# Performance work log

Measured on AMD Instinct MI355X. Metric: run time of the kernel, lower is better.

The kernel has to match this reference:

```python
import jax, jax.numpy as jnp
import numpy as np

CLIP = 10.0  # tanh clipping constant (Kool et al. C=10)


def setup_inputs() -> dict:
    key = jax.random.key(0)
    kq, kk, kv, km = jax.random.split(key, 4)
    B, M, N, D = 16, 2048, 2048, 128
    Q = jax.random.normal(kq, (B, M, D), dtype=jnp.float32)
    K = jax.random.normal(kk, (B, N, D), dtype=jnp.float32)
    V = jax.random.normal(kv, (B, N, D), dtype=jnp.float32)
    # mask: [B, N, 1] bool; True means "forbidden" (set logit to -inf).
    # p=0.3 so every row keeps plenty of valid keys (no all-masked rows).
    mask = jax.random.bernoulli(km, 0.3, (B, N, 1))
    return {"Q": Q, "K": K, "V": V, "mask": mask}


def reference(Q, K, V, mask):
    d_k = jnp.asarray(K.shape[-1], dtype=Q.dtype)
    # logits: [B, M, N]
    logits = jnp.einsum("bmd,bnd->bmn", Q, K) / jnp.sqrt(d_k)
    logits = CLIP * jnp.tanh(logits)
    # mask [B, N, 1] -> [B, 1, N], broadcast over query dim
    mask_t = jnp.transpose(mask, (0, 2, 1))
    logits = jnp.where(mask_t, -jnp.inf, logits)
    probs = jax.nn.softmax(logits, axis=-1)
    return jnp.einsum("bmn,bnd->bmd", probs, V)
```

## Files before the change

kernel.cpp:

```cpp
#include <hip/hip_runtime.h>
#include <hip/hip_fp16.h>

typedef _Float16 h8 __attribute__((ext_vector_type(8)));
typedef _Float16 h4 __attribute__((ext_vector_type(4)));
typedef float f32x4 __attribute__((ext_vector_type(4)));

#define MFMA16(a, b, c) __builtin_amdgcn_mfma_f32_16x16x32_f16((a), (b), (c), 0, 0, 0)

static constexpr int MM = 2048, NN = 2048, DD = 128;
static constexpr int MT = 64, KT = 64, NT = NN / KT;
static constexpr size_t KV_IMG = (size_t)16 * 32 * 16384;
static constexpr size_t WS_NEED = 2 * KV_IMG + 32768 * 4;

static constexpr float C1 = 0.25503487f;
static constexpr float C2 = 28.853900817779268f;
static constexpr float CVALID = 14.426950408889634f;
static constexpr float CMASK = -1.0e30f;

__device__ inline void glds16(const void* g, void* l) {
  __builtin_amdgcn_global_load_lds(
      (const __attribute__((address_space(1))) void*)g,
      (__attribute__((address_space(3))) void*)l, 16, 0, 0);
}

__global__ __launch_bounds__(256) void prep_all(
    const float* __restrict__ K, const float* __restrict__ V,
    const void* __restrict__ mraw, unsigned char* __restrict__ kimg,
    unsigned char* __restrict__ vimg, float* __restrict__ biasC) {
  const int id = blockIdx.x;
  const int tid = threadIdx.x;
  if (id >= 1024) {
    const unsigned int* mw = (const unsigned int*)mraw;
    const unsigned char* mb = (const unsigned char*)mraw;
    int okW = 1;
    for (int w = tid; w < 8192; w += 256) {
      unsigned int v = mw[w];
      okW &= (v == 0u || v == 1u || v == 0x3f800000u) ? 1 : 0;
    }
    __shared__ int sW;
    if (tid == 0) sW = 1;
    __syncthreads();
    if (!okW) atomicAnd(&sW, 0);
    __syncthreads();
    const int i = (id - 1024) * 256 + tid;
    bool masked = sW ? (mw[i] != 0u) : (mb[i] != 0);
    biasC[i] = masked ? CMASK : CVALID;
    return;
  }
  const int bt = id & 511;
  if (id < 512) {
    const float* src = K + (size_t)bt * KT * DD;
    unsigned char* dst = kimg + (size_t)bt * 16384;
#pragma unroll
    for (int it = 0; it < 4; ++it) {
      const int key = (tid >> 4) + 16 * it;
      const int o = tid & 15;
      f32x4 a = *(const f32x4*)(src + key * DD + 8 * o);
      f32x4 c = *(const f32x4*)(src + key * DD + 8 * o + 4);
      h8 hv;
#pragma unroll
      for (int j = 0; j < 4; ++j) {
        hv[j] = (_Float16)a[j];
        hv[j + 4] = (_Float16)c[j];
      }
      *(h8*)(dst + key * 256 + ((16 * o) ^ ((key & 7) << 4))) = hv;
    }
  } else {
    const float* src = V + (size_t)bt * KT * DD;
    unsigned char* dst = vimg + (size_t)bt * 16384;
    const int d = tid & 127;
    const int half = tid >> 7;
#pragma unroll
    for (int ki = 0; ki < 4; ++ki) {
      const int koct = half * 4 + ki;
      h8 w;
#pragma unroll
      for (int q = 0; q < 8; ++q)
        w[q] = (_Float16)src[(8 * koct + q) * DD + d];
      *(h8*)(dst + d * 128 + 16 * (koct ^ ((d >> 1) & 7))) = w;
    }
  }
}

__global__ __launch_bounds__(512, 4) void attn_main(
    const float* __restrict__ Qg, const unsigned char* __restrict__ kimg,
    const unsigned char* __restrict__ vimg, const float* __restrict__ biasC,
    float* __restrict__ out) {
  __shared__ __align__(16) unsigned char smem[76032];
  const int tid = threadIdx.x;
  const int lane = tid & 63;
  const int wv = tid >> 6;
  const int r = lane & 15;
  const int g = lane >> 4;
  const int rw = wv >> 1;
  const int h = wv & 1;
  const int bid = blockIdx.x;
  const int swz = ((bid & 7) << 6) | (bid >> 3);
  const int b = swz >> 5;
  const int mt = swz & 31;
  const int m0 = mt * MT + rw * 16;

  h8 qh[4];
  {
    const float* qr = Qg + ((size_t)b * MM + m0 + r) * DD;
#pragma unroll
    for (int t = 0; t < 4; ++t) {
      f32x4 a = *(const f32x4*)(qr + 32 * t + 8 * g);
      f32x4 c = *(const f32x4*)(qr + 32 * t + 8 * g + 4);
      h8 hi;
#pragma unroll
      for (int j = 0; j < 4; ++j) {
        hi[j] = (_Float16)a[j];
        hi[j + 4] = (_Float16)c[j];
      }
      qh[t] = hi;
    }
  }

  f32x4 acc[8];
#pragma unroll
  for (int cd = 0; cd < 8; ++cd) acc[cd] = (f32x4){0.f, 0.f, 0.f, 0.f};
  float rs[4] = {0.f, 0.f, 0.f, 0.f};

  const unsigned char* kib = kimg + (size_t)b * 32 * 16384;
  const unsigned char* vib = vimg + (size_t)b * 32 * 16384;
  const float* cb = biasC + b * NN;
  _Float16* plds = (_Float16*)(smem + 65536 + wv * 1280);

#pragma unroll
  for (int i = 0; i < 2; ++i) {
    const int off = wv * 2048 + i * 1024;
    glds16(kib + off + lane * 16, smem + off);
    glds16(vib + off + lane * 16, smem + 16384 + off);
  }
  __syncthreads();

  for (int tn = 0; tn < NT; ++tn) {
    const unsigned char* kbuf = smem + (tn & 1) * 32768;
    const unsigned char* vbuf = kbuf + 16384;
    if (tn + 1 < NT) {
      unsigned char* nbuf = smem + ((tn + 1) & 1) * 32768;
      const unsigned char* ks = kib + (size_t)(tn + 1) * 16384;
      const unsigned char* vs = vib + (size_t)(tn + 1) * 16384;
#pragma unroll
      for (int i = 0; i < 2; ++i) {
        const int off = wv * 2048 + i * 1024;
        glds16(ks + off + lane * 16, nbuf + off);
        glds16(vs + off + lane * 16, nbuf + 16384 + off);
      }
    }

#pragma unroll
    for (int c = 0; c < 2; ++c) {
      f32x4 S = {0.f, 0.f, 0.f, 0.f};
      const int key = h * 32 + 16 * c + r;
      const int krow = key << 8;
      const int ksw = (key & 7) << 4;
      __builtin_amdgcn_s_setprio(1);
#pragma unroll
      for (int t = 0; t < 4; ++t) {
        h8 kf = *(const h8*)(kbuf + krow + ((64 * t + 16 * g) ^ ksw));
        S = MFMA16(qh[t], kf, S);
      }
      __builtin_amdgcn_s_setprio(0);
      const float Cc = cb[tn * KT + key];
#pragma unroll
      for (int j = 0; j < 4; ++j) {
        float u = __builtin_amdgcn_exp2f(S[j] * C1);
        float p = __builtin_amdgcn_exp2f(
            fmaf(-C2, __builtin_amdgcn_rcpf(u + 1.0f), Cc));
        rs[j] += p;
        plds[(4 * g + j) * 40 + 16 * c + r] = (_Float16)p;
      }
    }
    h8 a0 = *(const h8*)((unsigned char*)plds + r * 80 + 16 * g);
    __builtin_amdgcn_s_setprio(1);
#pragma unroll
    for (int cd = 0; cd < 8; ++cd) {
      const int d = 16 * cd + r;
      h8 vf = *(const h8*)(vbuf + (d << 7) +
                           ((64 * h + 16 * g) ^ (((d >> 1) & 7) << 4)));
      acc[cd] = MFMA16(a0, vf, acc[cd]);
    }
    __builtin_amdgcn_s_setprio(0);
    __syncthreads();
  }

#pragma unroll
  for (int j = 0; j < 4; ++j) {
    float v = rs[j];
    v += __shfl_xor(v, 1);
    v += __shfl_xor(v, 2);
    v += __shfl_xor(v, 4);
    v += __shfl_xor(v, 8);
    rs[j] = v;
  }

  float* olds = (float*)smem;
  float* rslds = (float*)(smem + 75776);
  if (h == 1) {
    float* my = olds + rw * 2048;
#pragma unroll
    for (int cd = 0; cd < 8; ++cd)
#pragma unroll
      for (int j = 0; j < 4; ++j)
        my[(4 * g + j) * 128 + 16 * cd + r] = acc[cd][j];
    if (r == 0) {
#pragma unroll
      for (int j = 0; j < 4; ++j) rslds[rw * 16 + 4 * g + j] = rs[j];
    }
  }
  __syncthreads();
  if (h == 0) {
    const float* ot = olds + rw * 2048;
    float* ob = out + ((size_t)b * MM + m0) * DD;
#pragma unroll
    for (int j = 0; j < 4; ++j) {
      const int rl = 4 * g + j;
      const float tot = rs[j] + rslds[rw * 16 + rl];
      const float inv = __builtin_amdgcn_rcpf(tot);
#pragma unroll
      for (int cd = 0; cd < 8; ++cd) {
        float v = acc[cd][j] + ot[rl * 128 + 16 * cd + r];
        ob[rl * DD + 16 * cd + r] = v * inv;
      }
    }
  }
}

__global__ __launch_bounds__(256, 2) void attn_fallback(
    const float* __restrict__ Qg, const float* __restrict__ Kg,
    const float* __restrict__ Vg, const float* __restrict__ biasC,
    float* __restrict__ out) {
  __shared__ __align__(16) unsigned char smem[51456];
  const int tid = threadIdx.x;
  const int lane = tid & 63;
  const int wv = tid >> 6;
  const int r = lane & 15;
  const int g = lane >> 4;
  const int rw = wv >> 1;
  const int h = wv & 1;
  const int b = blockIdx.x >> 5;
  const int mt = blockIdx.x & 31;
  const int m0 = mt * MT + rw * 32;

  float* blds = (float*)(smem + 43264);
  {
    const float* cb = biasC + b * NN;
#pragma unroll
    for (int i = 0; i < 8; ++i) blds[tid + 256 * i] = cb[tid + 256 * i];
  }
  h8 qh[2][4];
  {
    const float* qb = Qg + ((size_t)b * MM + m0) * DD;
#pragma unroll
    for (int rf = 0; rf < 2; ++rf) {
      const float* qr = qb + (16 * rf + r) * DD;
#pragma unroll
      for (int t = 0; t < 4; ++t) {
        f32x4 a = *(const f32x4*)(qr + 32 * t + 8 * g);
        f32x4 c = *(const f32x4*)(qr + 32 * t + 8 * g + 4);
        h8 hi;
#pragma unroll
        for (int j = 0; j < 4; ++j) {
          hi[j] = (_Float16)a[j];
          hi[j + 4] = (_Float16)c[j];
        }
        qh[rf][t] = hi;
      }
    }
  }
  f32x4 acc[2][8];
#pragma unroll
  for (int rf = 0; rf < 2; ++rf)
#pragma unroll
    for (int cd = 0; cd < 8; ++cd) acc[rf][cd] = (f32x4){0.f, 0.f, 0.f, 0.f};
  float rs[2][4] = {{0.f, 0.f, 0.f, 0.f}, {0.f, 0.f, 0.f, 0.f}};
  const float* kb = Kg + (size_t)b * NN * DD;
  const float* vbp = Vg + (size_t)b * NN * DD;
  _Float16* plds = (_Float16*)(smem + 32768 + wv * 2560);
  const int bk0 = tid >> 5, bd0 = tid & 31;
  const int bk1 = (256 + tid) >> 5, bd1 = tid & 31;
  f32x4 kpre[8], vpre[8];
#pragma unroll
  for (int i = 0; i < 8; ++i) kpre[i] = *(const f32x4*)(kb + i * 1024 + tid * 4);
#pragma unroll
  for (int q = 0; q < 4; ++q) {
    vpre[q] = *(const f32x4*)(vbp + (4 * bk0 + q) * DD + 4 * bd0);
    vpre[4 + q] = *(const f32x4*)(vbp + (4 * bk1 + q) * DD + 4 * bd1);
  }
  for (int tn = 0; tn < NT; ++tn) {
#pragma unroll
    for (int i = 0; i < 8; ++i) {
      const int flat = i * 1024 + tid * 4;
      const int key = flat >> 7;
      const int d0 = flat & 127;
      h4 hv;
#pragma unroll
      for (int j = 0; j < 4; ++j) hv[j] = (_Float16)kpre[i][j];
      *(h4*)(smem + (key << 8) + ((d0 << 1) ^ ((key & 7) << 4))) = hv;
    }
#pragma unroll
    for (int it = 0; it < 2; ++it) {
      const int bk = it ? bk1 : bk0;
      const int bd = it ? bd1 : bd0;
#pragma unroll
      for (int p = 0; p < 4; ++p) {
        h4 w;
#pragma unroll
        for (int q = 0; q < 4; ++q) w[q] = (_Float16)vpre[it * 4 + q][p];
        const int d = 4 * bd + p;
        *(h4*)(smem + 16384 + (d << 7) +
               ((bk << 3) ^ (((d >> 1) & 7) << 4))) = w;
      }
    }
    if (tn + 1 < NT) {
      const float* ks = kb + (tn + 1) * KT * DD;
      const float* vs = vbp + (tn + 1) * KT * DD;
#pragma unroll
      for (int i = 0; i < 8; ++i) kpre[i] = *(const f32x4*)(ks + i * 1024 + tid * 4);
#pragma unroll
      for (int q = 0; q < 4; ++q) {
        vpre[q] = *(const f32x4*)(vs + (4 * bk0 + q) * DD + 4 * bd0);
        vpre[4 + q] = *(const f32x4*)(vs + (4 * bk1 + q) * DD + 4 * bd1);
      }
    }
    __syncthreads();
#pragma unroll
    for (int c = 0; c < 2; ++c) {
      f32x4 S0 = {0.f, 0.f, 0.f, 0.f}, S1 = {0.f, 0.f, 0.f, 0.f};
      const int key = h * 32 + 16 * c + r;
      const int krow = key << 8;
      const int ksw = (key & 7) << 4;
#pragma unroll
      for (int t = 0; t < 4; ++t) {
        h8 kf = *(const h8*)(smem + krow + ((64 * t + 16 * g) ^ ksw));
        S0 = MFMA16(qh[0][t], kf, S0);
        S1 = MFMA16(qh[1][t], kf, S1);
      }
      const float Cc = blds[tn * KT + key];
#pragma unroll
      for (int j = 0; j < 4; ++j) {
        float u0 = __builtin_amdgcn_exp2f(S0[j] * C1);
        float p0 = __builtin_amdgcn_exp2f(
            fmaf(-C2, __builtin_amdgcn_rcpf(u0 + 1.0f), Cc));
        rs[0][j] += p0;
        plds[(4 * g + j) * 40 + 16 * c + r] = (_Float16)p0;
        float u1 = __builtin_amdgcn_exp2f(S1[j] * C1);
        float p1 = __builtin_amdgcn_exp2f(
            fmaf(-C2, __builtin_amdgcn_rcpf(u1 + 1.0f), Cc));
        rs[1][j] += p1;
        plds[(16 + 4 * g + j) * 40 + 16 * c + r] = (_Float16)p1;
      }
    }
    h8 a0 = *(const h8*)((unsigned char*)plds + r * 80 + 16 * g);
    h8 a1 = *(const h8*)((unsigned char*)plds + (16 + r) * 80 + 16 * g);
#pragma unroll
    for (int cd = 0; cd < 8; ++cd) {
      const int d = 16 * cd + r;
      h8 vf = *(const h8*)(smem + 16384 + (d << 7) +
                           ((64 * h + 16 * g) ^ (((d >> 1) & 7) << 4)));
      acc[0][cd] = MFMA16(a0, vf, acc[0][cd]);
      acc[1][cd] = MFMA16(a1, vf, acc[1][cd]);
    }
    __syncthreads();
  }
#pragma unroll
  for (int rf = 0; rf < 2; ++rf)
#pragma unroll
    for (int j = 0; j < 4; ++j) {
      float v = rs[rf][j];
      v += __shfl_xor(v, 1);
      v += __shfl_xor(v, 2);
      v += __shfl_xor(v, 4);
      v += __shfl_xor(v, 8);
      rs[rf][j] = v;
    }
  float* olds = (float*)smem;
  float* rslds = (float*)(smem + 43008);
  if (h == 1) {
    float* my = olds + rw * 4096;
#pragma unroll
    for (int rf = 0; rf < 2; ++rf)
#pragma unroll
      for (int cd = 0; cd < 8; ++cd)
#pragma unroll
        for (int j = 0; j < 4; ++j)
          my[(16 * rf + 4 * g + j) * 128 + 16 * cd + r] = acc[rf][cd][j];
    if (r == 0) {
#pragma unroll
      for (int rf = 0; rf < 2; ++rf)
#pragma unroll
        for (int j = 0; j < 4; ++j)
          rslds[rw * 32 + 16 * rf + 4 * g + j] = rs[rf][j];
    }
  }
  __syncthreads();
  if (h == 0) {
    const float* ot = olds + rw * 4096;
    float* ob = out + ((size_t)b * MM + m0) * DD;
#pragma unroll
    for (int rf = 0; rf < 2; ++rf)
#pragma unroll
      for (int j = 0; j < 4; ++j) {
        const int rl = 16 * rf + 4 * g + j;
        const float tot = rs[rf][j] + rslds[rw * 32 + rl];
        const float inv = __builtin_amdgcn_rcpf(tot);
#pragma unroll
        for (int cd = 0; cd < 8; ++cd) {
          float v = acc[rf][cd][j] + ot[rl * 128 + 16 * cd + r];
          ob[rl * DD + 16 * cd + r] = v * inv;
        }
      }
  }
}

extern "C" void kernel_launch(void* const* d_in, const int* in_sizes, int n_in,
                              void* d_out, int out_size, void* d_ws, size_t ws_size,
                              hipStream_t stream) {
  const float* Q = (const float*)d_in[0];
  const float* K = (const float*)d_in[1];
  const float* V = (const float*)d_in[2];
  const void* mask = d_in[3];
  float* out = (float*)d_out;
  if (ws_size >= WS_NEED) {
    unsigned char* kimg = (unsigned char*)d_ws;
    unsigned char* vimg = kimg + KV_IMG;
    float* biasC = (float*)(kimg + 2 * KV_IMG);
    prep_all<<<dim3(1152), dim3(256), 0, stream>>>(K, V, mask, kimg, vimg, biasC);
    attn_main<<<dim3(512), dim3(512), 0, stream>>>(Q, kimg, vimg, biasC, out);
  } else {
    float* biasC = (float*)d_ws;
    prep_all<<<dim3(1152), dim3(256), 0, stream>>>(K, V, mask,
        (unsigned char*)d_ws, (unsigned char*)d_ws, biasC);
    attn_fallback<<<dim3(512), dim3(256), 0, stream>>>(Q, K, V, biasC, out);
  }
}
```

Baseline: 81.97 us.

## Switch attention main loop to 32x32x16 MFMA with 4-wave blocks

Rewrites the main attention kernel to use 32x32x16 MFMA tiles: each wave now owns 32 query rows and 32 keys per tile, with 256-thread blocks instead of 512. Row sums are computed with an MFMA against a ones vector instead of cross-lane shuffles, and the V image swizzle changes to match the new read pattern. This aims to cut LDS fragment reads and instruction overhead per FLOP, at the cost of more accumulator registers and fewer waves per block. The fallback path also gets a lighter bias-only prep kernel.

```diff
diff --git a/kernel.cpp b/kernel.cpp
--- a/kernel.cpp
+++ b/kernel.cpp
@@ -4,8 +4,10 @@
 typedef _Float16 h8 __attribute__((ext_vector_type(8)));
 typedef _Float16 h4 __attribute__((ext_vector_type(4)));
 typedef float f32x4 __attribute__((ext_vector_type(4)));
+typedef float f32x16 __attribute__((ext_vector_type(16)));
 
 #define MFMA16(a, b, c) __builtin_amdgcn_mfma_f32_16x16x32_f16((a), (b), (c), 0, 0, 0)
+#define MFMA32(a, b, c) __builtin_amdgcn_mfma_f32_32x32x16_f16((a), (b), (c), 0, 0, 0)
 
 static constexpr int MM = 2048, NN = 2048, DD = 128;
 static constexpr int MT = 64, KT = 64, NT = NN / KT;
@@ -21,6 +23,26 @@
   __builtin_amdgcn_global_load_lds(
       (const __attribute__((address_space(1))) void*)g,
       (__attribute__((address_space(3))) void*)l, 16, 0, 0);
+}
+
+__global__ __launch_bounds__(256) void prep_bias(const void* __restrict__ mraw,
+                                                 float* __restrict__ biasC) {
+  const int tid = threadIdx.x;
+  const unsigned int* mw = (const unsigned int*)mraw;
+  const unsigned char* mb = (const unsigned char*)mraw;
+  int okW = 1;
+  for (int w = tid; w < 8192; w += 256) {
+    unsigned int v = mw[w];
+    okW &= (v == 0u || v == 1u || v == 0x3f800000u) ? 1 : 0;
+  }
+  __shared__ int sW;
+  if (tid == 0) sW = 1;
+  __syncthreads();
+  if (!okW) atomicAnd(&sW, 0);
+  __syncthreads();
+  const int i = blockIdx.x * 256 + tid;
+  bool masked = sW ? (mw[i] != 0u) : (mb[i] != 0);
+  biasC[i] = masked ? CMASK : CVALID;
 }
 
 __global__ __launch_bounds__(256) void prep_all(
@@ -77,12 +99,12 @@
 #pragma unroll
       for (int q = 0; q < 8; ++q)
         w[q] = (_Float16)src[(8 * koct + q) * DD + d];
-      *(h8*)(dst + d * 128 + 16 * (koct ^ ((d >> 1) & 7))) = w;
-    }
-  }
-}
-
-__global__ __launch_bounds__(512, 4) void attn_main(
+      *(h8*)(dst + d * 128 + 16 * (koct ^ (d & 7))) = w;
+    }
+  }
+}
+
+__global__ __launch_bounds__(256, 2) void attn_main(
     const float* __restrict__ Qg, const unsigned char* __restrict__ kimg,
     const unsigned char* __restrict__ vimg, const float* __restrict__ biasC,
     float* __restrict__ out) {
@@ -90,50 +112,63 @@
   const int tid = threadIdx.x;
   const int lane = tid & 63;
   const int wv = tid >> 6;
-  const int r = lane & 15;
-  const int g = lane >> 4;
+  const int l31 = lane & 31;
+  const int hp = lane >> 5;
   const int rw = wv >> 1;
   const int h = wv & 1;
   const int bid = blockIdx.x;
   const int swz = ((bid & 7) << 6) | (bid >> 3);
   const int b = swz >> 5;
   const int mt = swz & 31;
-  const int m0 = mt * MT + rw * 16;
-
-  h8 qh[4];
+  const int m0 = mt * MT + rw * 32;
+
+  h8 qa[8];
   {
-    const float* qr = Qg + ((size_t)b * MM + m0 + r) * DD;
-#pragma unroll
-    for (int t = 0; t < 4; ++t) {
-      f32x4 a = *(const f32x4*)(qr + 32 * t + 8 * g);
-      f32x4 c = *(const f32x4*)(qr + 32 * t + 8 * g + 4);
+    const float* qr = Qg + ((size_t)b * MM + m0 + l31) * DD;
+#pragma unroll
+    for (int st = 0; st < 8; ++st) {
+      const int d0 = 16 * st + 8 * hp;
+      f32x4 a = *(const f32x4*)(qr + d0);
+      f32x4 c = *(const f32x4*)(qr + d0 + 4);
       h8 hi;
 #pragma unroll
       for (int j = 0; j < 4; ++j) {
         hi[j] = (_Float16)a[j];
         hi[j + 4] = (_Float16)c[j];
       }
-      qh[t] = hi;
-    }
-  }
-
-  f32x4 acc[8];
-#pragma unroll
-  for (int cd = 0; cd < 8; ++cd) acc[cd] = (f32x4){0.f, 0.f, 0.f, 0.f};
-  float rs[4] = {0.f, 0.f, 0.f, 0.f};
+      qa[st] = hi;
+    }
+  }
+
+  f32x16 oacc[4];
+  f32x16 rsacc;
+#pragma unroll
+  for (int dc = 0; dc < 4; ++dc)
+#pragma unroll
+    for (int j = 0; j < 16; ++j) oacc[dc][j] = 0.f;
+#pragma unroll
+  for (int j = 0; j < 16; ++j) rsacc[j] = 0.f;
+
+  h8 onesf;
+#pragma unroll
+  for (int j = 0; j < 8; ++j) onesf[j] = (_Float16)1.0f;
 
   const unsigned char* kib = kimg + (size_t)b * 32 * 16384;
   const unsigned char* vib = vimg + (size_t)b * 32 * 16384;
   const float* cb = biasC + b * NN;
-  _Float16* plds = (_Float16*)(smem + 65536 + wv * 1280);
-
-#pragma unroll
-  for (int i = 0; i < 2; ++i) {
-    const int off = wv * 2048 + i * 1024;
+  unsigned char* pscr = smem + 65536 + wv * 2560;
+
+#pragma unroll
+  for (int i = 0; i < 4; ++i) {
+    const int off = wv * 4096 + i * 1024;
     glds16(kib + off + lane * 16, smem + off);
     glds16(vib + off + lane * 16, smem + 16384 + off);
   }
   __syncthreads();
+
+  const int key = 32 * h + l31;
+  const int krow = key << 8;
+  const int ksw = (key & 7) << 4;
 
   for (int tn = 0; tn < NT; ++tn) {
     const unsigned char* kbuf = smem + (tn & 1) * 32768;
@@ -143,86 +178,77 @@
       const unsigned char* ks = kib + (size_t)(tn + 1) * 16384;
       const unsigned char* vs = vib + (size_t)(tn + 1) * 16384;
 #pragma unroll
-      for (int i = 0; i < 2; ++i) {
-        const int off = wv * 2048 + i * 1024;
+      for (int i = 0; i < 4; ++i) {
+        const int off = wv * 4096 + i * 1024;
         glds16(ks + off + lane * 16, nbuf + off);
         glds16(vs + off + lane * 16, nbuf + 16384 + off);
       }
     }
 
-#pragma unroll
-    for (int c = 0; c < 2; ++c) {
-      f32x4 S = {0.f, 0.f, 0.f, 0.f};
-      const int key = h * 32 + 16 * c + r;
-      const int krow = key << 8;
-      const int ksw = (key & 7) << 4;
-      __builtin_amdgcn_s_setprio(1);
-#pragma unroll
-      for (int t = 0; t < 4; ++t) {
-        h8 kf = *(const h8*)(kbuf + krow + ((64 * t + 16 * g) ^ ksw));
-        S = MFMA16(qh[t], kf, S);
-      }
-      __builtin_amdgcn_s_setprio(0);
-      const float Cc = cb[tn * KT + key];
-#pragma unroll
-      for (int j = 0; j < 4; ++j) {
-        float u = __builtin_amdgcn_exp2f(S[j] * C1);
-        float p = __builtin_amdgcn_exp2f(
-            fmaf(-C2, __builtin_amdgcn_rcpf(u + 1.0f), Cc));
-        rs[j] += p;
-        plds[(4 * g + j) * 40 + 16 * c + r] = (_Float16)p;
-      }
-    }
-    h8 a0 = *(const h8*)((unsigned char*)plds + r * 80 + 16 * g);
+    const float Cc = cb[tn * KT + key];
+
+    f32x16 s;
+#pragma unroll
+    for (int j = 0; j < 16; ++j) s[j] = 0.f;
     __builtin_amdgcn_s_setprio(1);
 #pragma unroll
-    for (int cd = 0; cd < 8; ++cd) {
-      const int d = 16 * cd + r;
-      h8 vf = *(const h8*)(vbuf + (d << 7) +
-                           ((64 * h + 16 * g) ^ (((d >> 1) & 7) << 4)));
-      acc[cd] = MFMA16(a0, vf, acc[cd]);
+    for (int st = 0; st < 8; ++st) {
+      h8 kf = *(const h8*)(kbuf + krow + ((32 * st + 16 * hp) ^ ksw));
+      s = MFMA32(qa[st], kf, s);
+    }
+    __builtin_amdgcn_s_setprio(0);
+
+#pragma unroll
+    for (int j = 0; j < 16; ++j) {
+      float u = __builtin_amdgcn_exp2f(s[j] * C1);
+      float p = __builtin_amdgcn_exp2f(
+          fmaf(-C2, __builtin_amdgcn_rcpf(u + 1.0f), Cc));
+      const int qrow = (j & 3) + 8 * (j >> 2) + 4 * hp;
+      *(_Float16*)(pscr + qrow * 80 + l31 * 2) = (_Float16)p;
+    }
+    h8 pa0 = *(const h8*)(pscr + l31 * 80 + 16 * hp);
+    h8 pa1 = *(const h8*)(pscr + l31 * 80 + 32 + 16 * hp);
+    __builtin_amdgcn_s_setprio(1);
+    rsacc = MFMA32(pa0, onesf, rsacc);
+    rsacc = MFMA32(pa1, onesf, rsacc);
+#pragma unroll
+    for (int dc = 0; dc < 4; ++dc) {
+      const int d = 32 * dc + l31;
+      const int vrow = d << 7;
+      const int vsw = (d & 7) << 4;
+      h8 vf0 = *(const h8*)(vbuf + vrow + ((64 * h + 16 * hp) ^ vsw));
+      h8 vf1 = *(const h8*)(vbuf + vrow + ((64 * h + 32 + 16 * hp) ^ vsw));
+      oacc[dc] = MFMA32(pa0, vf0, oacc[dc]);
+      oacc[dc] = MFMA32(pa1, vf1, oacc[dc]);
     }
     __builtin_amdgcn_s_setprio(0);
     __syncthreads();
-  }
-
-#pragma unroll
-  for (int j = 0; j < 4; ++j) {
-    float v = rs[j];
-    v += __shfl_xor(v, 1);
-    v += __shfl_xor(v, 2);
-    v += __shfl_xor(v, 4);
-    v += __shfl_xor(v, 8);
-    rs[j] = v;
   }
 
   float* olds = (float*)smem;
   float* rslds = (float*)(smem + 75776);
   if (h == 1) {
-    float* my = olds + rw * 2048;
-#pragma unroll
-    for (int cd = 0; cd < 8; ++cd)
-#pragma unroll
-      for (int j = 0; j < 4; ++j)
-        my[(4 * g + j) * 128 + 16 * cd + r] = acc[cd][j];
-    if (r == 0) {
-#pragma unroll
-      for (int j = 0; j < 4; ++j) rslds[rw * 16 + 4 * g + j] = rs[j];
+#pragma unroll
+    for (int j = 0; j < 16; ++j) {
+      const int qrow = (j & 3) + 8 * (j >> 2) + 4 * hp;
+#pragma unroll
+      for (int dc = 0; dc < 4; ++dc)
+        olds[(rw * 32 + qrow) * 128 + 32 * dc + l31] = oacc[dc][j];
+      if (l31 == 0) rslds[rw * 32 + qrow] = rsacc[j];
     }
   }
   __syncthreads();
   if (h == 0) {
-    const float* ot = olds + rw * 2048;
     float* ob = out + ((size_t)b * MM + m0) * DD;
 #pragma unroll
-    for (int j = 0; j < 4; ++j) {
-      const int rl = 4 * g + j;
-      const float tot = rs[j] + rslds[rw * 16 + rl];
+    for (int j = 0; j < 16; ++j) {
+      const int qrow = (j & 3) + 8 * (j >> 2) + 4 * hp;
+      const float tot = rsacc[j] + rslds[rw * 32 + qrow];
       const float inv = __builtin_amdgcn_rcpf(tot);
 #pragma unroll
-      for (int cd = 0; cd < 8; ++cd) {
-        float v = acc[cd][j] + ot[rl * 128 + 16 * cd + r];
-        ob[rl * DD + 16 * cd + r] = v * inv;
+      for (int dc = 0; dc < 4; ++dc) {
+        float v = oacc[dc][j] + olds[(rw * 32 + qrow) * 128 + 32 * dc + l31];
+        ob[qrow * DD + 32 * dc + l31] = v * inv;
       }
     }
   }
@@ -293,12 +319,12 @@
 #pragma unroll
     for (int i = 0; i < 8; ++i) {
       const int flat = i * 1024 + tid * 4;
-      const int key = flat >> 7;
+      const int kkey = flat >> 7;
       const int d0 = flat & 127;
       h4 hv;
 #pragma unroll
       for (int j = 0; j < 4; ++j) hv[j] = (_Float16)kpre[i][j];
-      *(h4*)(smem + (key << 8) + ((d0 << 1) ^ ((key & 7) << 4))) = hv;
+      *(h4*)(smem + (kkey << 8) + ((d0 << 1) ^ ((kkey & 7) << 4))) = hv;
     }
 #pragma unroll
     for (int it = 0; it < 2; ++it) {
@@ -329,16 +355,16 @@
 #pragma unroll
     for (int c = 0; c < 2; ++c) {
       f32x4 S0 = {0.f, 0.f, 0.f, 0.f}, S1 = {0.f, 0.f, 0.f, 0.f};
-      const int key = h * 32 + 16 * c + r;
-      const int krow = key << 8;
-      const int ksw = (key & 7) << 4;
+      const int kkey = h * 32 + 16 * c + r;
+      const int krow = kkey << 8;
+      const int ksw = (kkey & 7) << 4;
 #pragma unroll
       for (int t = 0; t < 4; ++t) {
         h8 kf = *(const h8*)(smem + krow + ((64 * t + 16 * g) ^ ksw));
         S0 = MFMA16(qh[0][t], kf, S0);
         S1 = MFMA16(qh[1][t], kf, S1);
       }
-      const float Cc = blds[tn * KT + key];
+      const float Cc = blds[tn * KT + kkey];
 #pragma unroll
       for (int j = 0; j < 4; ++j) {
         float u0 = __builtin_amdgcn_exp2f(S0[j] * C1);
@@ -428,11 +454,10 @@
     unsigned char* vimg = kimg + KV_IMG;
     float* biasC = (float*)(kimg + 2 * KV_IMG);
     prep_all<<<dim3(1152), dim3(256), 0, stream>>>(K, V, mask, kimg, vimg, biasC);
-    attn_main<<<dim3(512), dim3(512), 0, stream>>>(Q, kimg, vimg, biasC, out);
+    attn_main<<<dim3(512), dim3(256), 0, stream>>>(Q, kimg, vimg, biasC, out);
   } else {
     float* biasC = (float*)d_ws;
-    prep_all<<<dim3(1152), dim3(256), 0, stream>>>(K, V, mask,
-        (unsigned char*)d_ws, (unsigned char*)d_ws, biasC);
+    prep_bias<<<dim3(128), dim3(256), 0, stream>>>(mask, biasC);
     attn_fallback<<<dim3(512), dim3(256), 0, stream>>>(Q, K, V, biasC, out);
   }
 }
```

Result: no change. 82.41 us (+0.5%).
